# Performance work log

Hardware: AMD Instinct MI355X
Metric: run time of the kernel (lower is better)

## Reference

```python
import jax, jax.numpy as jnp
import numpy as np

B, S, H, D = 1, 2048, 16, 128
HID = H * D  # 2048
EPS = 1e-6


def setup_inputs() -> dict:
    key = jax.random.key(0)
    ks = jax.random.split(key, 6)
    sc = 1.0 / np.sqrt(HID)
    t = jnp.arange(S, dtype=jnp.float32)[:, None]
    inv = 1.0 / (10000.0 ** (jnp.arange(D // 2, dtype=jnp.float32) / (D // 2)))
    ang = t * inv[None, :]
    return {
        "hidden_states": jax.random.normal(ks[0], (B, S, HID), jnp.float32),
        "freqs_cos": jnp.cos(ang),
        "freqs_sin": jnp.sin(ang),
        "w_qkv": jax.random.normal(ks[1], (HID, 3 * HID), jnp.float32) * sc,
        "b_qkv": jnp.zeros((3 * HID,), jnp.float32),
        "w_norm_q": jnp.ones((HID,), jnp.float32),
        "w_norm_k": jnp.ones((HID,), jnp.float32),
        "w_out": jax.random.normal(ks[2], (HID, HID), jnp.float32) * sc,
        "b_out": jnp.zeros((HID,), jnp.float32),
    }


def _rmsnorm(x, w):
    var = jnp.mean(jnp.square(x), axis=-1, keepdims=True)
    return x * jax.lax.rsqrt(var + EPS) * w


def _rope(x, cos, sin):
    # x: [B, H, S, D]; cos/sin: [S, D//2], interleaved pair rotation
    xr = x.reshape(*x.shape[:-1], D // 2, 2)
    x1, x2 = xr[..., 0], xr[..., 1]
    c = cos[None, None, :, :]
    s = sin[None, None, :, :]
    o1 = x1 * c - x2 * s
    o2 = x1 * s + x2 * c
    return jnp.stack([o1, o2], axis=-1).reshape(x.shape)


def reference(hidden_states, freqs_cos, freqs_sin, w_qkv, b_qkv,
              w_norm_q, w_norm_k, w_out, b_out):
    qkv = hidden_states @ w_qkv + b_qkv  # [B, S, 3*HID]
    q, k, v = jnp.split(qkv, 3, axis=-1)
    q = _rmsnorm(q, w_norm_q).reshape(B, S, H, D).transpose(0, 2, 1, 3)
    k = _rmsnorm(k, w_norm_k).reshape(B, S, H, D).transpose(0, 2, 1, 3)
    v = v.reshape(B, S, H, D).transpose(0, 2, 1, 3)
    q = _rope(q, freqs_cos, freqs_sin)
    k = _rope(k, freqs_cos, freqs_sin)
    scale = 1.0 / np.sqrt(D)
    scores = jnp.einsum("bhqd,bhkd->bhqk", q, k) * scale
    attn = jax.nn.softmax(scores, axis=-1)
    out = jnp.einsum("bhqk,bhkd->bhqd", attn, v)
    out = out.transpose(0, 2, 1, 3).reshape(B, S, HID)
    return out @ w_out + b_out
```

## Files before the change

kernel.cpp:

```cpp
#include <hip/hip_runtime.h>
#include <math.h>

typedef unsigned short u16;
typedef __bf16 bf16x8 __attribute__((ext_vector_type(8)));
typedef float f32x4 __attribute__((ext_vector_type(4)));
typedef unsigned short u16x8 __attribute__((ext_vector_type(8)));

#define SLEN 2048
#define HIDN 2048
#define NH   16
#define DHD  128

static __device__ __forceinline__ float bf2f(u16 u) {
  unsigned int i = ((unsigned int)u) << 16;
  return __builtin_bit_cast(float, i);
}
static __device__ __forceinline__ u16 f2bf(float f) {
  unsigned int x = __builtin_bit_cast(unsigned int, f);
  unsigned int r = x + 0x7fffu + ((x >> 16) & 1u);
  return (u16)(r >> 16);
}
static __device__ __forceinline__ void gload_lds16(const u16* g, u16* l) {
  __builtin_amdgcn_global_load_lds((const __attribute__((address_space(1))) void*)g,
                                   (__attribute__((address_space(3))) void*)l,
                                   16, 0, 0);
}

__global__ __launch_bounds__(256) void transpcvt(const float* __restrict__ in,
                                                 u16* __restrict__ out,
                                                 int istride, int ostride) {
  __shared__ float tl[64][65];
  const int t = threadIdx.x;
  const int r0 = blockIdx.x * 64, c0 = blockIdx.y * 64;
#pragma unroll
  for (int it = 0; it < 4; ++it) {
    int row = it * 16 + (t >> 4);
    int col = (t & 15) * 4;
    f32x4 v = *(const f32x4*)&in[(size_t)(r0 + row) * istride + c0 + col];
    tl[row][col] = v[0]; tl[row][col + 1] = v[1];
    tl[row][col + 2] = v[2]; tl[row][col + 3] = v[3];
  }
  __syncthreads();
#pragma unroll
  for (int it = 0; it < 2; ++it) {
    int orow = it * 32 + (t >> 3);
    int ocol = (t & 7) * 8;
    u16x8 v;
#pragma unroll
    for (int j = 0; j < 8; ++j) v[j] = f2bf(tl[ocol + j][orow]);
    *(u16x8*)&out[(size_t)(c0 + orow) * ostride + r0 + ocol] = v;
  }
}

__global__ __launch_bounds__(256) void cvt_bf16(const float* __restrict__ in,
                                                u16* __restrict__ out) {
  int i = (blockIdx.x * 256 + threadIdx.x) * 8;
  f32x4 a = *(const f32x4*)&in[i];
  f32x4 b = *(const f32x4*)&in[i + 4];
  u16x8 v;
#pragma unroll
  for (int j = 0; j < 4; ++j) { v[j] = f2bf(a[j]); v[4 + j] = f2bf(b[j]); }
  *(u16x8*)&out[i] = v;
}

__global__ __launch_bounds__(256) void transp(const u16* __restrict__ in,
                                              u16* __restrict__ out,
                                              int istride, int ostride,
                                              int in_z, int out_z) {
  in  += (size_t)blockIdx.z * in_z;
  out += (size_t)blockIdx.z * out_z;
  __shared__ u16 tl[64][72];
  const int t  = threadIdx.x;
  const int r0 = blockIdx.x * 64, c0 = blockIdx.y * 64;
#pragma unroll
  for (int it = 0; it < 2; ++it) {
    int row = it * 32 + (t >> 3);
    int col = (t & 7) * 8;
    *(u16x8*)&tl[row][col] =
        *(const u16x8*)&in[(size_t)(r0 + row) * istride + c0 + col];
  }
  __syncthreads();
#pragma unroll
  for (int it = 0; it < 2; ++it) {
    int orow = it * 32 + (t >> 3);
    int ocol = (t & 7) * 8;
    u16x8 v;
#pragma unroll
    for (int j = 0; j < 8; ++j) v[j] = tl[ocol + j][orow];
    *(u16x8*)&out[(size_t)(c0 + orow) * ostride + r0 + ocol] = v;
  }
}

__global__ __launch_bounds__(256) void gemm_bt(const u16* __restrict__ A,
                                               const u16* __restrict__ BT,
                                               const float* __restrict__ bias,
                                               float* Cf, u16* Cb,
                                               int M, int N, int K) {
  __shared__ u16 lA[128 * 64];
  __shared__ u16 lB[128 * 64];
  const int t = threadIdx.x;
  const int lane = t & 63, w = t >> 6;
  const int g = lane >> 4, l16 = lane & 15;
  const int wr = w >> 1, wc = w & 1;
  const u16* Ab = A + (size_t)blockIdx.x * 128 * K;
  const u16* Bb = BT + (size_t)blockIdx.y * 128 * K;

  f32x4 acc[4][4];
#pragma unroll
  for (int mi = 0; mi < 4; ++mi)
#pragma unroll
    for (int ni = 0; ni < 4; ++ni) acc[mi][ni] = (f32x4)(0.0f);

  for (int k0 = 0; k0 < K; k0 += 64) {
    __syncthreads();
#pragma unroll
    for (int i = 0; i < 4; ++i) {
      int e = t * 8 + i * 2048;
      int row = e >> 6;
      int col16 = (e & 63) >> 3;
      int scol = (col16 ^ (row & 7)) * 8;
      gload_lds16(Ab + (size_t)row * K + k0 + scol, &lA[e]);
      gload_lds16(Bb + (size_t)row * K + k0 + scol, &lB[e]);
    }
    __syncthreads();
#pragma unroll
    for (int kk = 0; kk < 2; ++kk) {
      bf16x8 af[4], bfr[4];
#pragma unroll
      for (int mi = 0; mi < 4; ++mi) {
        int row = wr * 64 + mi * 16 + l16;
        af[mi] = *(const bf16x8*)&lA[row * 64 + (((4 * kk + g) ^ (l16 & 7)) << 3)];
      }
#pragma unroll
      for (int ni = 0; ni < 4; ++ni) {
        int row = wc * 64 + ni * 16 + l16;
        bfr[ni] = *(const bf16x8*)&lB[row * 64 + (((4 * kk + g) ^ (l16 & 7)) << 3)];
      }
#pragma unroll
      for (int mi = 0; mi < 4; ++mi)
#pragma unroll
        for (int ni = 0; ni < 4; ++ni)
          acc[mi][ni] = __builtin_amdgcn_mfma_f32_16x16x32_bf16(af[mi], bfr[ni],
                                                                acc[mi][ni], 0, 0, 0);
    }
  }

#pragma unroll
  for (int ni = 0; ni < 4; ++ni) {
    int n = blockIdx.y * 128 + wc * 64 + ni * 16 + l16;
    float bv = bias[n];
#pragma unroll
    for (int mi = 0; mi < 4; ++mi) {
      int m = blockIdx.x * 128 + wr * 64 + mi * 16 + 4 * g;
#pragma unroll
      for (int r = 0; r < 4; ++r) {
        float v = acc[mi][ni][r] + bv;
        if (Cf) Cf[(size_t)(m + r) * N + n] = v;
        else    Cb[(size_t)(m + r) * N + n] = f2bf(v);
      }
    }
  }
}

__global__ __launch_bounds__(256) void rms_rope(const u16* __restrict__ qkv,
                                                const float* __restrict__ fcos,
                                                const float* __restrict__ fsin,
                                                const float* __restrict__ wq,
                                                const float* __restrict__ wk,
                                                u16* __restrict__ Qr,
                                                u16* __restrict__ Kr) {
  const int s = blockIdx.x;
  const int t = threadIdx.x;
  const int lane = t & 63, w = t >> 6;
  __shared__ float red[2][4];
  const u16* row = qkv + (size_t)s * (3 * HIDN);

  u16x8 xq = *(const u16x8*)&row[t * 8];
  u16x8 xk = *(const u16x8*)&row[HIDN + t * 8];
  float fq[8], fk[8];
  float ssq = 0.f, ssk = 0.f;
#pragma unroll
  for (int j = 0; j < 8; ++j) {
    fq[j] = bf2f(xq[j]); ssq += fq[j] * fq[j];
    fk[j] = bf2f(xk[j]); ssk += fk[j] * fk[j];
  }
#pragma unroll
  for (int off = 32; off >= 1; off >>= 1) {
    ssq += __shfl_xor(ssq, off);
    ssk += __shfl_xor(ssk, off);
  }
  if (lane == 0) { red[0][w] = ssq; red[1][w] = ssk; }
  __syncthreads();
  float sq = red[0][0] + red[0][1] + red[0][2] + red[0][3];
  float sk = red[1][0] + red[1][1] + red[1][2] + red[1][3];
  float rq = rsqrtf(sq / (float)HIDN + 1e-6f);
  float rk = rsqrtf(sk / (float)HIDN + 1e-6f);

  f32x4 wq0 = *(const f32x4*)&wq[t * 8];
  f32x4 wq1 = *(const f32x4*)&wq[t * 8 + 4];
  f32x4 wk0 = *(const f32x4*)&wk[t * 8];
  f32x4 wk1 = *(const f32x4*)&wk[t * 8 + 4];
  float wqa[8] = {wq0[0], wq0[1], wq0[2], wq0[3], wq1[0], wq1[1], wq1[2], wq1[3]};
  float wka[8] = {wk0[0], wk0[1], wk0[2], wk0[3], wk1[0], wk1[1], wk1[2], wk1[3]};
  const int c0 = t * 8;
  const int h = c0 >> 7;
  const int d0 = c0 & 127;
  const int i0 = d0 >> 1;
  const float* cp = fcos + (size_t)s * (DHD / 2) + i0;
  const float* sp = fsin + (size_t)s * (DHD / 2) + i0;
  const float qscale = 0.08838834764831845f;

  u16x8 oq, ok;
#pragma unroll
  for (int p = 0; p < 4; ++p) {
    float c = cp[p], sn = sp[p];
    float q1 = fq[2 * p] * rq * wqa[2 * p];
    float q2 = fq[2 * p + 1] * rq * wqa[2 * p + 1];
    float k1 = fk[2 * p] * rk * wka[2 * p];
    float k2 = fk[2 * p + 1] * rk * wka[2 * p + 1];
    oq[2 * p]     = f2bf((q1 * c - q2 * sn) * qscale);
    oq[2 * p + 1] = f2bf((q1 * sn + q2 * c) * qscale);
    ok[2 * p]     = f2bf(k1 * c - k2 * sn);
    ok[2 * p + 1] = f2bf(k1 * sn + k2 * c);
  }
  size_t o = (size_t)h * SLEN * DHD + (size_t)s * DHD + d0;
  *(u16x8*)&Qr[o] = oq;
  *(u16x8*)&Kr[o] = ok;
}

__global__ __launch_bounds__(256) void attn_fwd(const u16* __restrict__ Qr,
                                                const u16* __restrict__ Kr,
                                                const u16* __restrict__ Vt,
                                                u16* __restrict__ out) {
  const int lin = blockIdx.x;
  const int xcd = lin & 7, idx = lin >> 3;
  const int h = xcd + ((idx >> 5) << 3);
  const int qb = idx & 31;
  const int t = threadIdx.x;
  const int lane = t & 63, w = t >> 6;
  const int g = lane >> 4, l16 = lane & 15;
  const int q0 = qb * 64 + w * 16;
  const u16* Qh = Qr + (size_t)h * SLEN * DHD;
  const u16* Kh = Kr + (size_t)h * SLEN * DHD;
  const u16* Vh = Vt + (size_t)h * DHD * SLEN;

  __shared__ u16 Kl[2][64 * 128];
  __shared__ u16 Vl[2][128 * 64];
  __shared__ u16 Pl[4][16][72];

  bf16x8 aq[4];
#pragma unroll
  for (int dk = 0; dk < 4; ++dk)
    aq[dk] = *(const bf16x8*)&Qh[(size_t)(q0 + l16) * DHD + dk * 32 + g * 8];

  f32x4 o[8];
#pragma unroll
  for (int df = 0; df < 8; ++df) o[df] = (f32x4)(0.0f);
  float m[4], lsum[4];
#pragma unroll
  for (int r = 0; r < 4; ++r) { m[r] = -INFINITY; lsum[r] = 0.f; }

#pragma unroll
  for (int i = 0; i < 4; ++i) {
    int e = t * 8 + i * 2048;
    int kr = e >> 7, kc = (e & 127) >> 3;
    gload_lds16(Kh + (size_t)kr * DHD + ((kc ^ (kr & 7)) << 3), &Kl[0][e]);
    int vr = e >> 6, vc = (e & 63) >> 3;
    gload_lds16(Vh + (size_t)vr * SLEN + ((vc ^ (vr & 7)) << 3), &Vl[0][e]);
  }
  __syncthreads();

  int cur = 0;
  for (int kt = 0; kt < SLEN / 64; ++kt) {
    if (kt + 1 < SLEN / 64) {
      const int kv1 = (kt + 1) * 64;
#pragma unroll
      for (int i = 0; i < 4; ++i) {
        int e = t * 8 + i * 2048;
        int kr = e >> 7, kc = (e & 127) >> 3;
        gload_lds16(Kh + (size_t)(kv1 + kr) * DHD + ((kc ^ (kr & 7)) << 3),
                    &Kl[cur ^ 1][e]);
        int vr = e >> 6, vc = (e & 63) >> 3;
        gload_lds16(Vh + (size_t)vr * SLEN + kv1 + ((vc ^ (vr & 7)) << 3),
                    &Vl[cur ^ 1][e]);
      }
    }

    f32x4 s4[4];
#pragma unroll
    for (int nf = 0; nf < 4; ++nf) s4[nf] = (f32x4)(0.0f);
#pragma unroll
    for (int nf = 0; nf < 4; ++nf) {
#pragma unroll
      for (int dk = 0; dk < 4; ++dk) {
        bf16x8 bk = *(const bf16x8*)&Kl[cur][(nf * 16 + l16) * 128 +
                                            (((dk * 4 + g) ^ (l16 & 7)) << 3)];
        s4[nf] = __builtin_amdgcn_mfma_f32_16x16x32_bf16(aq[dk], bk, s4[nf], 0, 0, 0);
      }
    }
    float tm[4];
#pragma unroll
    for (int r = 0; r < 4; ++r) {
      tm[r] = s4[0][r];
#pragma unroll
      for (int nf = 1; nf < 4; ++nf) tm[r] = fmaxf(tm[r], s4[nf][r]);
    }
#pragma unroll
    for (int off = 1; off < 16; off <<= 1)
#pragma unroll
      for (int r = 0; r < 4; ++r) tm[r] = fmaxf(tm[r], __shfl_xor(tm[r], off));
    float corr[4], ts[4];
#pragma unroll
    for (int r = 0; r < 4; ++r) {
      float mn = fmaxf(m[r], tm[r]);
      corr[r] = __expf(m[r] - mn);
      m[r] = mn;
      ts[r] = 0.f;
    }
#pragma unroll
    for (int nf = 0; nf < 4; ++nf)
#pragma unroll
      for (int r = 0; r < 4; ++r) {
        float p = __expf(s4[nf][r] - m[r]);
        s4[nf][r] = p;
        ts[r] += p;
      }
#pragma unroll
    for (int off = 1; off < 16; off <<= 1)
#pragma unroll
      for (int r = 0; r < 4; ++r) ts[r] += __shfl_xor(ts[r], off);
#pragma unroll
    for (int r = 0; r < 4; ++r) lsum[r] = lsum[r] * corr[r] + ts[r];
#pragma unroll
    for (int df = 0; df < 8; ++df)
#pragma unroll
      for (int r = 0; r < 4; ++r) o[df][r] *= corr[r];
#pragma unroll
    for (int nf = 0; nf < 4; ++nf)
#pragma unroll
      for (int r = 0; r < 4; ++r)
        Pl[w][4 * g + r][nf * 16 + l16] = f2bf(s4[nf][r]);
#pragma unroll
    for (int ks = 0; ks < 2; ++ks) {
      bf16x8 ap = *(const bf16x8*)&Pl[w][l16][ks * 32 + g * 8];
#pragma unroll
      for (int df = 0; df < 8; ++df) {
        bf16x8 bv = *(const bf16x8*)&Vl[cur][(df * 16 + l16) * 64 +
                                             (((ks * 4 + g) ^ (l16 & 7)) << 3)];
        o[df] = __builtin_amdgcn_mfma_f32_16x16x32_bf16(ap, bv, o[df], 0, 0, 0);
      }
    }
    __syncthreads();
    cur ^= 1;
  }

  float inv[4];
#pragma unroll
  for (int r = 0; r < 4; ++r) inv[r] = 1.0f / lsum[r];
#pragma unroll
  for (int df = 0; df < 8; ++df)
#pragma unroll
    for (int r = 0; r < 4; ++r)
      out[(size_t)(q0 + 4 * g + r) * HIDN + h * DHD + df * 16 + l16] =
          f2bf(o[df][r] * inv[r]);
}

extern "C" void kernel_launch(void* const* d_in, const int* in_sizes, int n_in,
                              void* d_out, int out_size, void* d_ws, size_t ws_size,
                              hipStream_t stream) {
  (void)in_sizes; (void)n_in; (void)out_size; (void)ws_size;
  const float* hs   = (const float*)d_in[0];
  const float* fc   = (const float*)d_in[1];
  const float* fs   = (const float*)d_in[2];
  const float* wqkv = (const float*)d_in[3];
  const float* bqkv = (const float*)d_in[4];
  const float* wnq  = (const float*)d_in[5];
  const float* wnk  = (const float*)d_in[6];
  const float* wout = (const float*)d_in[7];
  const float* bout = (const float*)d_in[8];
  float* out = (float*)d_out;
  char* ws = (char*)d_ws;

  u16* wqkvT = (u16*)(ws);
  u16* woutT = (u16*)(ws + 25165824);
  u16* qkv   = (u16*)(ws + 33554432);
  u16* hsB   = (u16*)(ws + 58720256);
  u16* Qr    = (u16*)(ws + 58720256);
  u16* Kr    = (u16*)(ws + 67108864);
  u16* Vt    = (u16*)(ws + 75497472);
  u16* attnO = (u16*)(ws + 83886080);

  transpcvt<<<dim3(32, 96), 256, 0, stream>>>(wqkv, wqkvT, 6144, 2048);
  transpcvt<<<dim3(32, 32), 256, 0, stream>>>(wout, woutT, 2048, 2048);
  cvt_bf16<<<dim3(2048), 256, 0, stream>>>(hs, hsB);
  gemm_bt<<<dim3(16, 48), 256, 0, stream>>>(hsB, wqkvT, bqkv, nullptr, qkv,
                                            2048, 6144, 2048);
  rms_rope<<<dim3(2048), 256, 0, stream>>>(qkv, fc, fs, wnq, wnk, Qr, Kr);
  transp<<<dim3(32, 2, 16), 256, 0, stream>>>(qkv + 4096, Vt, 6144, 2048, 128, 262144);
  attn_fwd<<<dim3(512), 256, 0, stream>>>(Qr, Kr, Vt, attnO);
  gemm_bt<<<dim3(16, 16), 256, 0, stream>>>(attnO, woutT, bout, out, nullptr,
                                            2048, 2048, 2048);
}
```

Before: 229.5 us.

## Transpose score MFMA, fold log2e into Q scale, skip rescale when max unchanged

Swaps the MFMA operands for QK^T so each lane holds one query row's scores. The row max and sum then need only two cross-lane shuffles instead of four rounds over four rows. The log2(e) factor is folded into the Q scale so exp2f replaces __expf. Rescaling of the output accumulator is skipped when no row's max grew across the whole wave, and the P store layout is changed to match the transposed scores. Correction and inverse-sum values are redistributed with __shfl, which adds some lane-mapping complexity and correctness risk.

```diff
diff --git a/kernel.cpp b/kernel.cpp
--- a/kernel.cpp
+++ b/kernel.cpp
@@ -208,7 +208,7 @@
   const int i0 = d0 >> 1;
   const float* cp = fcos + (size_t)s * (DHD / 2) + i0;
   const float* sp = fsin + (size_t)s * (DHD / 2) + i0;
-  const float qscale = 0.08838834764831845f;
+  const float qscale = 0.12751744925f;
 
   u16x8 oq, ok;
 #pragma unroll
@@ -256,9 +256,7 @@
   f32x4 o[8];
 #pragma unroll
   for (int df = 0; df < 8; ++df) o[df] = (f32x4)(0.0f);
-  float m[4], lsum[4];
-#pragma unroll
-  for (int r = 0; r < 4; ++r) { m[r] = -INFINITY; lsum[r] = 0.f; }
+  float m = -INFINITY, lsum = 0.f;
 
 #pragma unroll
   for (int i = 0; i < 4; ++i) {
@@ -295,51 +293,47 @@
       for (int dk = 0; dk < 4; ++dk) {
         bf16x8 bk = *(const bf16x8*)&Kl[cur][(nf * 16 + l16) * 128 +
                                             (((dk * 4 + g) ^ (l16 & 7)) << 3)];
-        s4[nf] = __builtin_amdgcn_mfma_f32_16x16x32_bf16(aq[dk], bk, s4[nf], 0, 0, 0);
-      }
-    }
-    float tm[4];
-#pragma unroll
-    for (int r = 0; r < 4; ++r) {
-      tm[r] = s4[0][r];
-#pragma unroll
-      for (int nf = 1; nf < 4; ++nf) tm[r] = fmaxf(tm[r], s4[nf][r]);
-    }
-#pragma unroll
-    for (int off = 1; off < 16; off <<= 1)
-#pragma unroll
-      for (int r = 0; r < 4; ++r) tm[r] = fmaxf(tm[r], __shfl_xor(tm[r], off));
-    float corr[4], ts[4];
-#pragma unroll
-    for (int r = 0; r < 4; ++r) {
-      float mn = fmaxf(m[r], tm[r]);
-      corr[r] = __expf(m[r] - mn);
-      m[r] = mn;
-      ts[r] = 0.f;
-    }
+        s4[nf] = __builtin_amdgcn_mfma_f32_16x16x32_bf16(bk, aq[dk], s4[nf], 0, 0, 0);
+      }
+    }
+    float tm = s4[0][0];
 #pragma unroll
     for (int nf = 0; nf < 4; ++nf)
 #pragma unroll
+      for (int r = 0; r < 4; ++r) tm = fmaxf(tm, s4[nf][r]);
+    tm = fmaxf(tm, __shfl_xor(tm, 16));
+    tm = fmaxf(tm, __shfl_xor(tm, 32));
+    const bool nogrow = (tm <= m);
+    const float mn = nogrow ? m : tm;
+    float ls = 0.f;
+#pragma unroll
+    for (int nf = 0; nf < 4; ++nf)
+#pragma unroll
       for (int r = 0; r < 4; ++r) {
-        float p = __expf(s4[nf][r] - m[r]);
+        float p = exp2f(s4[nf][r] - mn);
         s4[nf][r] = p;
-        ts[r] += p;
-      }
-#pragma unroll
-    for (int off = 1; off < 16; off <<= 1)
-#pragma unroll
-      for (int r = 0; r < 4; ++r) ts[r] += __shfl_xor(ts[r], off);
-#pragma unroll
-    for (int r = 0; r < 4; ++r) lsum[r] = lsum[r] * corr[r] + ts[r];
-#pragma unroll
-    for (int df = 0; df < 8; ++df)
-#pragma unroll
-      for (int r = 0; r < 4; ++r) o[df][r] *= corr[r];
+        ls += p;
+      }
+    ls += __shfl_xor(ls, 16);
+    ls += __shfl_xor(ls, 32);
+    if (__all(nogrow)) {
+      lsum += ls;
+    } else {
+      float corr = exp2f(m - mn);
+      m = mn;
+      lsum = lsum * corr + ls;
+#pragma unroll
+      for (int r = 0; r < 4; ++r) {
+        float cr = __shfl(corr, 20 * g + r);
+#pragma unroll
+        for (int df = 0; df < 8; ++df) o[df][r] *= cr;
+      }
+    }
 #pragma unroll
     for (int nf = 0; nf < 4; ++nf)
 #pragma unroll
       for (int r = 0; r < 4; ++r)
-        Pl[w][4 * g + r][nf * 16 + l16] = f2bf(s4[nf][r]);
+        Pl[w][l16][nf * 16 + 4 * g + r] = f2bf(s4[nf][r]);
 #pragma unroll
     for (int ks = 0; ks < 2; ++ks) {
       bf16x8 ap = *(const bf16x8*)&Pl[w][l16][ks * 32 + g * 8];
@@ -354,15 +348,15 @@
     cur ^= 1;
   }
 
-  float inv[4];
-#pragma unroll
-  for (int r = 0; r < 4; ++r) inv[r] = 1.0f / lsum[r];
-#pragma unroll
-  for (int df = 0; df < 8; ++df)
-#pragma unroll
-    for (int r = 0; r < 4; ++r)
+  const float invq = 1.0f / lsum;
+#pragma unroll
+  for (int r = 0; r < 4; ++r) {
+    float ir = __shfl(invq, 20 * g + r);
+#pragma unroll
+    for (int df = 0; df < 8; ++df)
       out[(size_t)(q0 + 4 * g + r) * HIDN + h * DHD + df * 16 + l16] =
-          f2bf(o[df][r] * inv[r]);
+          f2bf(o[df][r] * ir);
+  }
 }
 
 extern "C" void kernel_launch(void* const* d_in, const int* in_sizes, int n_in,
```

New measurement: 214.2 us. 1.07x faster.
